# Performance work log

Measured on AMD Instinct MI355X. Metric: run time of the kernel, lower is better.

## Reference

```python
import jax, jax.numpy as jnp
import numpy as np
from jax import lax

NUM_EXPERTS = 64
HIDDEN = 1024
INTERMEDIATE = 768
TOTAL_TOKENS = 8192


def setup_inputs() -> dict:
    key = jax.random.key(0)
    k1, k2, k3, k4 = jax.random.split(key, 4)
    x = jax.random.normal(k1, (TOTAL_TOKENS, HIDDEN), dtype=jnp.float32)
    scale = 0.02
    w1 = jax.random.normal(k2, (NUM_EXPERTS, HIDDEN, INTERMEDIATE), dtype=jnp.float32) * scale
    w2 = jax.random.normal(k3, (NUM_EXPERTS, INTERMEDIATE, HIDDEN), dtype=jnp.float32) * scale
    w3 = jax.random.normal(k4, (NUM_EXPERTS, HIDDEN, INTERMEDIATE), dtype=jnp.float32) * scale
    # Variable tokens per expert, summing exactly to TOTAL_TOKENS (tokens are pre-sorted by expert).
    counts = np.random.default_rng(0).multinomial(TOTAL_TOKENS, [1.0 / NUM_EXPERTS] * NUM_EXPERTS)
    num_tokens_per_expert = jnp.asarray(counts, dtype=jnp.int32)
    return {"x": x, "w1": w1, "w2": w2, "w3": w3,
            "num_tokens_per_expert": num_tokens_per_expert}


def reference(x, w1, w2, w3, num_tokens_per_expert):
    """SwiGLU grouped-expert FFN: down(silu(gate(x)) * up(x)), grouped by expert.

    x: (T, H) tokens sorted by expert; num_tokens_per_expert: (E,) int32.
    Matches torch._grouped_mm semantics: compute in bfloat16, cast back to x.dtype.
    """
    gs = num_tokens_per_expert.astype(jnp.int32)
    xb = x.astype(jnp.bfloat16)
    w1b = w1.astype(jnp.bfloat16)
    w2b = w2.astype(jnp.bfloat16)
    w3b = w3.astype(jnp.bfloat16)
    gate = lax.ragged_dot(xb, w1b, gs)          # (T, I) grouped GEMM
    up = lax.ragged_dot(xb, w3b, gs)            # (T, I)
    h = jax.nn.silu(gate) * up                  # fused SwiGLU activation
    out = lax.ragged_dot(h, w2b, gs)            # (T, H)
    return out.astype(x.dtype)
```

## Files before the change

kernel.cpp:

```cpp
#include <hip/hip_runtime.h>
#include <stdint.h>

#define E_ 64
#define H_ 1024
#define I_ 768
#define T_ 8192

typedef __attribute__((ext_vector_type(4))) float floatx4;
typedef __attribute__((ext_vector_type(8))) short bf16x8;

__device__ inline unsigned short f2bf(float f) {
  union { float f; uint32_t u; } v; v.f = f;
  return (unsigned short)((v.u + 0x7FFFu + ((v.u >> 16) & 1u)) >> 16);
}
__device__ inline float bf2f(unsigned short s) {
  union { uint32_t u; float f; } v; v.u = ((uint32_t)s) << 16;
  return v.f;
}

__device__ inline void gload16(const void* g, void* l) {
  __builtin_amdgcn_global_load_lds(
      (const __attribute__((address_space(1))) void*)g,
      (__attribute__((address_space(3))) void*)l, 16, 0, 0);
}

__device__ inline int bslot(int n, int c) { return n * 4 + (c ^ ((n >> 1) & 3)); }

__global__ void k_prep(const float* __restrict__ x, unsigned short* __restrict__ xb,
                       const int* __restrict__ cnts, int* __restrict__ offs) {
  int i = blockIdx.x * 256 + threadIdx.x;
  float4 v = ((const float4*)x)[i];
  ushort4 o;
  o.x = f2bf(v.x); o.y = f2bf(v.y); o.z = f2bf(v.z); o.w = f2bf(v.w);
  ((ushort4*)xb)[i] = o;
  if (i == 0) {
    int s = 0; offs[0] = 0;
    for (int e = 0; e < E_; ++e) { s += cnts[e]; offs[e + 1] = s; }
  }
}

__global__ __launch_bounds__(256, 2) void k_gemm1(
    const unsigned short* __restrict__ xb, const float* __restrict__ w1,
    const float* __restrict__ w3, unsigned short* __restrict__ h,
    const int* __restrict__ offs) {
  __shared__ __align__(16) float Bf[2][2][32 * 64];
  __shared__ __align__(16) unsigned short Bh[2][64 * 32];

  const int tid = threadIdx.x;
  const int wv = tid >> 6;
  const int l = tid & 63;
  const int lq = l >> 4;
  const int ln = l & 15;
  const int bid = ((int)blockIdx.x & 7) * (E_ * (I_ / 64) / 8) + ((int)blockIdx.x >> 3);
  const int e = bid / (I_ / 64);
  const int n0 = (bid % (I_ / 64)) * 64;
  const int off = offs[e];
  const int cnt = offs[e + 1] - off;

  const int cn = tid & 63;
  const int ck = tid >> 6;

  const float* b1p = w1 + (size_t)e * (H_ * I_) + (size_t)(tid >> 4) * I_ + n0 + (tid & 15) * 4;
  const float* b3p = w3 + (size_t)e * (H_ * I_) + (size_t)(tid >> 4) * I_ + n0 + (tid & 15) * 4;

  for (int mb = 0; mb < cnt; mb += 256) {
    const int m_here = (cnt - mb) < 256 ? (cnt - mb) : 256;
    const bool active = (wv * 64) < m_here;

    const unsigned short* aF[4];
#pragma unroll
    for (int mf = 0; mf < 4; ++mf) {
      int row = off + mb + wv * 64 + mf * 16 + ln;
      row = row < (T_ - 1) ? row : (T_ - 1);
      aF[mf] = xb + (size_t)row * H_ + lq * 8;
    }

    auto STGB = [&](int kt, int buf) {
#pragma unroll
      for (int r = 0; r < 2; ++r) {
        gload16(b1p + (size_t)(kt * 32 + r * 16) * I_, &Bf[buf][0][tid * 4 + r * 1024]);
        gload16(b3p + (size_t)(kt * 32 + r * 16) * I_, &Bf[buf][1][tid * 4 + r * 1024]);
      }
    };

    floatx4 accG[4][4], accU[4][4];
#pragma unroll
    for (int i2 = 0; i2 < 4; ++i2)
#pragma unroll
      for (int j2 = 0; j2 < 4; ++j2) {
        accG[i2][j2] = (floatx4){0.f, 0.f, 0.f, 0.f};
        accU[i2][j2] = (floatx4){0.f, 0.f, 0.f, 0.f};
      }

    const int NK = H_ / 32;
    STGB(0, 0);
    STGB(1, 1);
    for (int kt = 0; kt < NK; ++kt) {
      const int cur = kt & 1;
      if (kt == NK - 1) asm volatile("s_waitcnt vmcnt(0)" ::: "memory");
      else              asm volatile("s_waitcnt vmcnt(4)" ::: "memory");
      __builtin_amdgcn_s_barrier();
      asm volatile("" ::: "memory");

#pragma unroll
      for (int m = 0; m < 2; ++m) {
        uint32_t dw[4];
#pragma unroll
        for (int d = 0; d < 4; ++d) {
          float v0 = Bf[cur][m][(ck * 8 + 2 * d) * 64 + cn];
          float v1 = Bf[cur][m][(ck * 8 + 2 * d + 1) * 64 + cn];
          dw[d] = (uint32_t)f2bf(v0) | ((uint32_t)f2bf(v1) << 16);
        }
        *(uint4*)&Bh[m][(size_t)bslot(cn, ck) * 8] = make_uint4(dw[0], dw[1], dw[2], dw[3]);
      }
      asm volatile("s_waitcnt lgkmcnt(0)" ::: "memory");
      __builtin_amdgcn_s_barrier();
      asm volatile("" ::: "memory");

      bf16x8 af[4];
      if (active) {
#pragma unroll
        for (int mf = 0; mf < 4; ++mf) af[mf] = *(const bf16x8*)(aF[mf] + kt * 32);
      }
      asm volatile("" ::: "memory");
      if (kt + 2 < NK) STGB(kt + 2, cur);
      asm volatile("" ::: "memory");

      if (active) {
        bf16x8 bG[4], bU[4];
#pragma unroll
        for (int nf = 0; nf < 4; ++nf) {
          const int sl = bslot(nf * 16 + ln, lq) * 8;
          bG[nf] = *(const bf16x8*)&Bh[0][sl];
          bU[nf] = *(const bf16x8*)&Bh[1][sl];
        }
#pragma unroll
        for (int mf = 0; mf < 4; ++mf)
#pragma unroll
          for (int nf = 0; nf < 4; ++nf) {
            accG[mf][nf] = __builtin_amdgcn_mfma_f32_16x16x32_bf16(af[mf], bG[nf], accG[mf][nf], 0, 0, 0);
            accU[mf][nf] = __builtin_amdgcn_mfma_f32_16x16x32_bf16(af[mf], bU[nf], accU[mf][nf], 0, 0, 0);
          }
      }
    }

    if (active) {
#pragma unroll
      for (int mf = 0; mf < 4; ++mf)
#pragma unroll
        for (int nf = 0; nf < 4; ++nf)
#pragma unroll
          for (int r = 0; r < 4; ++r) {
            int row_l = wv * 64 + mf * 16 + lq * 4 + r;
            if (row_l < m_here) {
              float g = bf2f(f2bf(accG[mf][nf][r]));
              float u = bf2f(f2bf(accU[mf][nf][r]));
              float hv = (g / (1.0f + __expf(-g))) * u;
              h[(size_t)(off + mb + row_l) * I_ + n0 + nf * 16 + ln] = f2bf(hv);
            }
          }
    }
    asm volatile("s_waitcnt vmcnt(0)" ::: "memory");
  }
}

__global__ __launch_bounds__(256, 3) void k_gemm2(
    const unsigned short* __restrict__ h, const float* __restrict__ w2,
    float* __restrict__ out, const int* __restrict__ offs) {
  __shared__ __align__(16) float Bf[2][32 * 64];
  __shared__ __align__(16) unsigned short Bh[64 * 32];

  const int tid = threadIdx.x;
  const int wv = tid >> 6;
  const int l = tid & 63;
  const int lq = l >> 4;
  const int ln = l & 15;
  const int bid = ((int)blockIdx.x & 7) * (E_ * (H_ / 64) / 8) + ((int)blockIdx.x >> 3);
  const int e = bid / (H_ / 64);
  const int n0 = (bid % (H_ / 64)) * 64;
  const int off = offs[e];
  const int cnt = offs[e + 1] - off;

  const int cn = tid & 63;
  const int ck = tid >> 6;

  const float* b2p = w2 + (size_t)e * (I_ * H_) + (size_t)(tid >> 4) * H_ + n0 + (tid & 15) * 4;

  for (int mb = 0; mb < cnt; mb += 256) {
    const int m_here = (cnt - mb) < 256 ? (cnt - mb) : 256;
    const bool active = (wv * 64) < m_here;

    const unsigned short* aF[4];
#pragma unroll
    for (int mf = 0; mf < 4; ++mf) {
      int row = off + mb + wv * 64 + mf * 16 + ln;
      row = row < (T_ - 1) ? row : (T_ - 1);
      aF[mf] = h + (size_t)row * I_ + lq * 8;
    }

    auto STGB = [&](int kt, int buf) {
#pragma unroll
      for (int r = 0; r < 2; ++r)
        gload16(b2p + (size_t)(kt * 32 + r * 16) * H_, &Bf[buf][tid * 4 + r * 1024]);
    };

    floatx4 acc[4][4];
#pragma unroll
    for (int i2 = 0; i2 < 4; ++i2)
#pragma unroll
      for (int j2 = 0; j2 < 4; ++j2) acc[i2][j2] = (floatx4){0.f, 0.f, 0.f, 0.f};

    const int NK = I_ / 32;
    STGB(0, 0);
    STGB(1, 1);
    for (int kt = 0; kt < NK; ++kt) {
      const int cur = kt & 1;
      if (kt == NK - 1) asm volatile("s_waitcnt vmcnt(0)" ::: "memory");
      else              asm volatile("s_waitcnt vmcnt(2)" ::: "memory");
      __builtin_amdgcn_s_barrier();
      asm volatile("" ::: "memory");

      {
        uint32_t dw[4];
#pragma unroll
        for (int d = 0; d < 4; ++d) {
          float v0 = Bf[cur][(ck * 8 + 2 * d) * 64 + cn];
          float v1 = Bf[cur][(ck * 8 + 2 * d + 1) * 64 + cn];
          dw[d] = (uint32_t)f2bf(v0) | ((uint32_t)f2bf(v1) << 16);
        }
        *(uint4*)&Bh[(size_t)bslot(cn, ck) * 8] = make_uint4(dw[0], dw[1], dw[2], dw[3]);
      }
      asm volatile("s_waitcnt lgkmcnt(0)" ::: "memory");
      __builtin_amdgcn_s_barrier();
      asm volatile("" ::: "memory");

      bf16x8 af[4];
      if (active) {
#pragma unroll
        for (int mf = 0; mf < 4; ++mf) af[mf] = *(const bf16x8*)(aF[mf] + kt * 32);
      }
      asm volatile("" ::: "memory");
      if (kt + 2 < NK) STGB(kt + 2, cur);
      asm volatile("" ::: "memory");

      if (active) {
        bf16x8 bF[4];
#pragma unroll
        for (int nf = 0; nf < 4; ++nf)
          bF[nf] = *(const bf16x8*)&Bh[(size_t)bslot(nf * 16 + ln, lq) * 8];
#pragma unroll
        for (int mf = 0; mf < 4; ++mf)
#pragma unroll
          for (int nf = 0; nf < 4; ++nf)
            acc[mf][nf] = __builtin_amdgcn_mfma_f32_16x16x32_bf16(af[mf], bF[nf], acc[mf][nf], 0, 0, 0);
      }
    }

    if (active) {
#pragma unroll
      for (int mf = 0; mf < 4; ++mf)
#pragma unroll
        for (int nf = 0; nf < 4; ++nf)
#pragma unroll
          for (int r = 0; r < 4; ++r) {
            int row_l = wv * 64 + mf * 16 + lq * 4 + r;
            if (row_l < m_here)
              out[(size_t)(off + mb + row_l) * H_ + n0 + nf * 16 + ln] = acc[mf][nf][r];
          }
    }
    asm volatile("s_waitcnt vmcnt(0)" ::: "memory");
  }
}

extern "C" void kernel_launch(void* const* d_in, const int* in_sizes, int n_in,
                              void* d_out, int out_size, void* d_ws, size_t ws_size,
                              hipStream_t stream) {
  const float* x  = (const float*)d_in[0];
  const float* w1 = (const float*)d_in[1];
  const float* w2 = (const float*)d_in[2];
  const float* w3 = (const float*)d_in[3];
  const int* cnts = (const int*)d_in[4];
  float* out = (float*)d_out;

  char* ws = (char*)d_ws;
  int* offs = (int*)ws;
  unsigned short* xb = (unsigned short*)(ws + 1024);
  unsigned short* h  = (unsigned short*)(ws + 1024 + (size_t)T_ * H_ * 2);

  k_prep<<<(T_ * H_) / (256 * 4), 256, 0, stream>>>(x, xb, cnts, offs);
  k_gemm1<<<E_ * (I_ / 64), 256, 0, stream>>>(xb, w1, w3, h, offs);
  k_gemm2<<<E_ * (H_ / 64), 256, 0, stream>>>(h, w2, out, offs);
}
```

Baseline: 619.3 us.

## Pre-convert weights to bf16 tiled layout and pipeline GEMMs with 4-stage buffers

A new prep kernel converts x to bf16 and also converts w1, w3 and w2 to bf16, written in an MFMA-ready tiled layout in workspace. The GEMM kernels then DMA bf16 tiles directly into a 4-deep LDS ring, with no in-loop fp32-to-bf16 conversion, only one barrier per k-step, and A fragments prefetched one step ahead. The goal is to remove per-tile conversion and LDS round trips from the GEMM inner loop. The cost is an extra pass that reads all fp32 weights and writes bf16 copies on every call, and a large workspace; if the workspace is too small, the old path runs.

```diff
diff --git a/kernel.cpp b/kernel.cpp
--- a/kernel.cpp
+++ b/kernel.cpp
@@ -24,20 +24,257 @@
       (__attribute__((address_space(3))) void*)l, 16, 0, 0);
 }
 
+__global__ void k_pt(const float* __restrict__ x, unsigned short* __restrict__ xb,
+                     const int* __restrict__ cnts, int* __restrict__ offs,
+                     const float* __restrict__ w1, const float* __restrict__ w3,
+                     const float* __restrict__ w2, unsigned short* __restrict__ w1t,
+                     unsigned short* __restrict__ w3t, unsigned short* __restrict__ w2t) {
+  const int tid = threadIdx.x;
+  const int b = blockIdx.x;
+  if (b < 8192) {
+    int i = b * 256 + tid;
+    float4 v = ((const float4*)x)[i];
+    ushort4 o;
+    o.x = f2bf(v.x); o.y = f2bf(v.y); o.z = f2bf(v.z); o.w = f2bf(v.w);
+    ((ushort4*)xb)[i] = o;
+    if (i == 0) {
+      int s = 0; offs[0] = 0;
+      for (int e = 0; e < E_; ++e) { s += cnts[e]; offs[e + 1] = s; }
+    }
+    return;
+  }
+  const int t2 = b - 8192;
+  const float* srcp; unsigned short* dstp; int N, KT, NB, idx;
+  if (t2 < 2048)      { srcp = w1; dstp = w1t; N = I_; KT = 32; NB = 12; idx = t2; }
+  else if (t2 < 4096) { srcp = w3; dstp = w3t; N = I_; KT = 32; NB = 12; idx = t2 - 2048; }
+  else                { srcp = w2; dstp = w2t; N = H_; KT = 24; NB = 16; idx = t2 - 4096; }
+  const int e = idx / KT, kt = idx % KT;
+  const int K = KT * 32;
+  const float* s0 = srcp + (size_t)e * K * N + (size_t)(kt * 32 + (tid & 3) * 8) * N + (tid >> 2);
+  unsigned short* d0 = dstp + ((size_t)e * NB * KT + kt) * 2048 + (size_t)tid * 8;
+  for (int nb = 0; nb < NB; ++nb) {
+    const float* s = s0 + nb * 64;
+    uint32_t dw[4];
+#pragma unroll
+    for (int d2 = 0; d2 < 4; ++d2) {
+      float v0 = s[(size_t)(2 * d2) * N];
+      float v1 = s[(size_t)(2 * d2 + 1) * N];
+      dw[d2] = (uint32_t)f2bf(v0) | ((uint32_t)f2bf(v1) << 16);
+    }
+    *(uint4*)(d0 + (size_t)nb * KT * 2048) = make_uint4(dw[0], dw[1], dw[2], dw[3]);
+  }
+}
+
+__global__ __launch_bounds__(256, 2) void k_gemm1_t(
+    const unsigned short* __restrict__ xb, const unsigned short* __restrict__ w1t,
+    const unsigned short* __restrict__ w3t, unsigned short* __restrict__ h,
+    const int* __restrict__ offs) {
+  __shared__ __align__(16) unsigned short Bh[4][2][2048];
+
+  const int tid = threadIdx.x;
+  const int wv = tid >> 6;
+  const int l = tid & 63;
+  const int lq = l >> 4;
+  const int ln = l & 15;
+  const int bid = ((int)blockIdx.x & 7) * (E_ * (I_ / 64) / 8) + ((int)blockIdx.x >> 3);
+  const int e = bid / (I_ / 64);
+  const int nb = bid % (I_ / 64);
+  const int n0 = nb * 64;
+  const int off = offs[e];
+  const int cnt = offs[e + 1] - off;
+
+  const unsigned short* w1s = w1t + (size_t)(e * 12 + nb) * (32 * 2048);
+  const unsigned short* w3s = w3t + (size_t)(e * 12 + nb) * (32 * 2048);
+  const int dmaOff = wv * 512 + l * 8;
+
+#define STGB1(kt)                                                            \
+  do {                                                                       \
+    int _b = (kt) & 3;                                                       \
+    gload16(w1s + (size_t)(kt) * 2048 + dmaOff, &Bh[_b][0][dmaOff]);         \
+    gload16(w3s + (size_t)(kt) * 2048 + dmaOff, &Bh[_b][1][dmaOff]);         \
+  } while (0)
+
+  for (int mb = 0; mb < cnt; mb += 256) {
+    const int m_here = (cnt - mb) < 256 ? (cnt - mb) : 256;
+    const bool active = (wv * 64) < m_here;
+
+    const unsigned short* aF[4];
+#pragma unroll
+    for (int mf = 0; mf < 4; ++mf) {
+      int row = off + mb + wv * 64 + mf * 16 + ln;
+      row = row < (T_ - 1) ? row : (T_ - 1);
+      aF[mf] = xb + (size_t)row * H_ + lq * 8;
+    }
+
+    floatx4 accG[4][4], accU[4][4];
+#pragma unroll
+    for (int i2 = 0; i2 < 4; ++i2)
+#pragma unroll
+      for (int j2 = 0; j2 < 4; ++j2) {
+        accG[i2][j2] = (floatx4){0.f, 0.f, 0.f, 0.f};
+        accU[i2][j2] = (floatx4){0.f, 0.f, 0.f, 0.f};
+      }
+
+    STGB1(0);
+    STGB1(1);
+    bf16x8 afA[4], afB[4];
+#pragma unroll
+    for (int mf = 0; mf < 4; ++mf) afA[mf] = *(const bf16x8*)(aF[mf]);
+
+#define STEP1(kt, cons, pref)                                                  \
+  do {                                                                         \
+    if ((kt) + 2 < 32) STGB1((kt) + 2);                                        \
+    if ((kt) + 1 < 32) {                                                       \
+      _Pragma("unroll") for (int mf = 0; mf < 4; ++mf)                         \
+          pref[mf] = *(const bf16x8*)(aF[mf] + ((kt) + 1) * 32);               \
+    }                                                                          \
+    asm volatile("s_waitcnt vmcnt(6)" ::: "memory");                           \
+    __builtin_amdgcn_s_barrier();                                              \
+    asm volatile("" ::: "memory");                                             \
+    const unsigned short* B0 = Bh[(kt) & 3][0];                                \
+    const unsigned short* B1 = Bh[(kt) & 3][1];                                \
+    if (active) {                                                              \
+      bf16x8 bG[4], bU[4];                                                     \
+      _Pragma("unroll") for (int nf = 0; nf < 4; ++nf) {                       \
+        int sl = ((nf * 16 + ln) * 4 + lq) * 8;                                \
+        bG[nf] = *(const bf16x8*)&B0[sl];                                      \
+        bU[nf] = *(const bf16x8*)&B1[sl];                                      \
+      }                                                                        \
+      _Pragma("unroll") for (int mf = 0; mf < 4; ++mf)                         \
+          _Pragma("unroll") for (int nf = 0; nf < 4; ++nf) {                   \
+        accG[mf][nf] =                                                         \
+            __builtin_amdgcn_mfma_f32_16x16x32_bf16(cons[mf], bG[nf],          \
+                                                    accG[mf][nf], 0, 0, 0);    \
+        accU[mf][nf] =                                                         \
+            __builtin_amdgcn_mfma_f32_16x16x32_bf16(cons[mf], bU[nf],          \
+                                                    accU[mf][nf], 0, 0, 0);    \
+      }                                                                        \
+    }                                                                          \
+    asm volatile("" ::: "memory");                                             \
+  } while (0)
+
+    for (int kt = 0; kt < 32; kt += 2) {
+      STEP1(kt, afA, afB);
+      STEP1(kt + 1, afB, afA);
+    }
+
+    if (active) {
+#pragma unroll
+      for (int mf = 0; mf < 4; ++mf)
+#pragma unroll
+        for (int nf = 0; nf < 4; ++nf)
+#pragma unroll
+          for (int r = 0; r < 4; ++r) {
+            int row_l = wv * 64 + mf * 16 + lq * 4 + r;
+            if (row_l < m_here) {
+              float g = bf2f(f2bf(accG[mf][nf][r]));
+              float u = bf2f(f2bf(accU[mf][nf][r]));
+              float hv = (g / (1.0f + __expf(-g))) * u;
+              h[(size_t)(off + mb + row_l) * I_ + n0 + nf * 16 + ln] = f2bf(hv);
+            }
+          }
+    }
+    asm volatile("s_waitcnt vmcnt(0)" ::: "memory");
+    __builtin_amdgcn_s_barrier();
+  }
+#undef STEP1
+#undef STGB1
+}
+
+__global__ __launch_bounds__(256, 2) void k_gemm2_t(
+    const unsigned short* __restrict__ h, const unsigned short* __restrict__ w2t,
+    float* __restrict__ out, const int* __restrict__ offs) {
+  __shared__ __align__(16) unsigned short Bh[4][2048];
+
+  const int tid = threadIdx.x;
+  const int wv = tid >> 6;
+  const int l = tid & 63;
+  const int lq = l >> 4;
+  const int ln = l & 15;
+  const int bid = ((int)blockIdx.x & 7) * (E_ * (H_ / 64) / 8) + ((int)blockIdx.x >> 3);
+  const int e = bid / (H_ / 64);
+  const int nb = bid % (H_ / 64);
+  const int n0 = nb * 64;
+  const int off = offs[e];
+  const int cnt = offs[e + 1] - off;
+
+  const unsigned short* w2s = w2t + (size_t)(e * 16 + nb) * (24 * 2048);
+  const int dmaOff = wv * 512 + l * 8;
+
+#define STGB2(kt) gload16(w2s + (size_t)(kt) * 2048 + dmaOff, &Bh[(kt) & 3][dmaOff])
+
+  for (int mb = 0; mb < cnt; mb += 256) {
+    const int m_here = (cnt - mb) < 256 ? (cnt - mb) : 256;
+    const bool active = (wv * 64) < m_here;
+
+    const unsigned short* aF[4];
+#pragma unroll
+    for (int mf = 0; mf < 4; ++mf) {
+      int row = off + mb + wv * 64 + mf * 16 + ln;
+      row = row < (T_ - 1) ? row : (T_ - 1);
+      aF[mf] = h + (size_t)row * I_ + lq * 8;
+    }
+
+    floatx4 acc[4][4];
+#pragma unroll
+    for (int i2 = 0; i2 < 4; ++i2)
+#pragma unroll
+      for (int j2 = 0; j2 < 4; ++j2) acc[i2][j2] = (floatx4){0.f, 0.f, 0.f, 0.f};
+
+    STGB2(0);
+    STGB2(1);
+    bf16x8 afA[4], afB[4];
+#pragma unroll
+    for (int mf = 0; mf < 4; ++mf) afA[mf] = *(const bf16x8*)(aF[mf]);
+
+#define STEP2(kt, cons, pref)                                                  \
+  do {                                                                         \
+    if ((kt) + 2 < 24) STGB2((kt) + 2);                                        \
+    if ((kt) + 1 < 24) {                                                       \
+      _Pragma("unroll") for (int mf = 0; mf < 4; ++mf)                         \
+          pref[mf] = *(const bf16x8*)(aF[mf] + ((kt) + 1) * 32);               \
+    }                                                                          \
+    asm volatile("s_waitcnt vmcnt(5)" ::: "memory");                           \
+    __builtin_amdgcn_s_barrier();                                              \
+    asm volatile("" ::: "memory");                                             \
+    const unsigned short* B0 = Bh[(kt) & 3];                                   \
+    if (active) {                                                              \
+      bf16x8 bF[4];                                                            \
+      _Pragma("unroll") for (int nf = 0; nf < 4; ++nf)                         \
+          bF[nf] = *(const bf16x8*)&B0[((nf * 16 + ln) * 4 + lq) * 8];         \
+      _Pragma("unroll") for (int mf = 0; mf < 4; ++mf)                         \
+          _Pragma("unroll") for (int nf = 0; nf < 4; ++nf)                     \
+              acc[mf][nf] = __builtin_amdgcn_mfma_f32_16x16x32_bf16(           \
+                  cons[mf], bF[nf], acc[mf][nf], 0, 0, 0);                     \
+    }                                                                          \
+    asm volatile("" ::: "memory");                                             \
+  } while (0)
+
+    for (int kt = 0; kt < 24; kt += 2) {
+      STEP2(kt, afA, afB);
+      STEP2(kt + 1, afB, afA);
+    }
+
+    if (active) {
+#pragma unroll
+      for (int mf = 0; mf < 4; ++mf)
+#pragma unroll
+        for (int nf = 0; nf < 4; ++nf)
+#pragma unroll
+          for (int r = 0; r < 4; ++r) {
+            int row_l = wv * 64 + mf * 16 + lq * 4 + r;
+            if (row_l < m_here)
+              out[(size_t)(off + mb + row_l) * H_ + n0 + nf * 16 + ln] = acc[mf][nf][r];
+          }
+    }
+    asm volatile("s_waitcnt vmcnt(0)" ::: "memory");
+    __builtin_amdgcn_s_barrier();
+  }
+#undef STEP2
+#undef STGB2
+}
+
 __device__ inline int bslot(int n, int c) { return n * 4 + (c ^ ((n >> 1) & 3)); }
-
-__global__ void k_prep(const float* __restrict__ x, unsigned short* __restrict__ xb,
-                       const int* __restrict__ cnts, int* __restrict__ offs) {
-  int i = blockIdx.x * 256 + threadIdx.x;
-  float4 v = ((const float4*)x)[i];
-  ushort4 o;
-  o.x = f2bf(v.x); o.y = f2bf(v.y); o.z = f2bf(v.z); o.w = f2bf(v.w);
-  ((ushort4*)xb)[i] = o;
-  if (i == 0) {
-    int s = 0; offs[0] = 0;
-    for (int e = 0; e < E_; ++e) { s += cnts[e]; offs[e + 1] = s; }
-  }
-}
 
 __global__ __launch_bounds__(256, 2) void k_gemm1(
     const unsigned short* __restrict__ xb, const float* __restrict__ w1,
@@ -56,17 +293,14 @@
   const int n0 = (bid % (I_ / 64)) * 64;
   const int off = offs[e];
   const int cnt = offs[e + 1] - off;
-
   const int cn = tid & 63;
   const int ck = tid >> 6;
-
   const float* b1p = w1 + (size_t)e * (H_ * I_) + (size_t)(tid >> 4) * I_ + n0 + (tid & 15) * 4;
   const float* b3p = w3 + (size_t)e * (H_ * I_) + (size_t)(tid >> 4) * I_ + n0 + (tid & 15) * 4;
 
   for (int mb = 0; mb < cnt; mb += 256) {
     const int m_here = (cnt - mb) < 256 ? (cnt - mb) : 256;
     const bool active = (wv * 64) < m_here;
-
     const unsigned short* aF[4];
 #pragma unroll
     for (int mf = 0; mf < 4; ++mf) {
@@ -74,7 +308,6 @@
       row = row < (T_ - 1) ? row : (T_ - 1);
       aF[mf] = xb + (size_t)row * H_ + lq * 8;
     }
-
     auto STGB = [&](int kt, int buf) {
 #pragma unroll
       for (int r = 0; r < 2; ++r) {
@@ -82,7 +315,6 @@
         gload16(b3p + (size_t)(kt * 32 + r * 16) * I_, &Bf[buf][1][tid * 4 + r * 1024]);
       }
     };
-
     floatx4 accG[4][4], accU[4][4];
 #pragma unroll
     for (int i2 = 0; i2 < 4; ++i2)
@@ -91,7 +323,6 @@
         accG[i2][j2] = (floatx4){0.f, 0.f, 0.f, 0.f};
         accU[i2][j2] = (floatx4){0.f, 0.f, 0.f, 0.f};
       }
-
     const int NK = H_ / 32;
     STGB(0, 0);
     STGB(1, 1);
@@ -101,7 +332,6 @@
       else              asm volatile("s_waitcnt vmcnt(4)" ::: "memory");
       __builtin_amdgcn_s_barrier();
       asm volatile("" ::: "memory");
-
 #pragma unroll
       for (int m = 0; m < 2; ++m) {
         uint32_t dw[4];
@@ -116,7 +346,6 @@
       asm volatile("s_waitcnt lgkmcnt(0)" ::: "memory");
       __builtin_amdgcn_s_barrier();
       asm volatile("" ::: "memory");
-
       bf16x8 af[4];
       if (active) {
 #pragma unroll
@@ -125,7 +354,6 @@
       asm volatile("" ::: "memory");
       if (kt + 2 < NK) STGB(kt + 2, cur);
       asm volatile("" ::: "memory");
-
       if (active) {
         bf16x8 bG[4], bU[4];
 #pragma unroll
@@ -143,7 +371,6 @@
           }
       }
     }
-
     if (active) {
 #pragma unroll
       for (int mf = 0; mf < 4; ++mf)
@@ -164,7 +391,7 @@
   }
 }
 
-__global__ __launch_bounds__(256, 3) void k_gemm2(
+__global__ __launch_bounds__(256, 2) void k_gemm2(
     const unsigned short* __restrict__ h, const float* __restrict__ w2,
     float* __restrict__ out, const int* __restrict__ offs) {
   __shared__ __align__(16) float Bf[2][32 * 64];
@@ -180,16 +407,13 @@
   const int n0 = (bid % (H_ / 64)) * 64;
   const int off = offs[e];
   const int cnt = offs[e + 1] - off;
-
   const int cn = tid & 63;
   const int ck = tid >> 6;
-
   const float* b2p = w2 + (size_t)e * (I_ * H_) + (size_t)(tid >> 4) * H_ + n0 + (tid & 15) * 4;
 
   for (int mb = 0; mb < cnt; mb += 256) {
     const int m_here = (cnt - mb) < 256 ? (cnt - mb) : 256;
     const bool active = (wv * 64) < m_here;
-
     const unsigned short* aF[4];
 #pragma unroll
     for (int mf = 0; mf < 4; ++mf) {
@@ -197,19 +421,16 @@
       row = row < (T_ - 1) ? row : (T_ - 1);
       aF[mf] = h + (size_t)row * I_ + lq * 8;
     }
-
     auto STGB = [&](int kt, int buf) {
 #pragma unroll
       for (int r = 0; r < 2; ++r)
         gload16(b2p + (size_t)(kt * 32 + r * 16) * H_, &Bf[buf][tid * 4 + r * 1024]);
     };
-
     floatx4 acc[4][4];
 #pragma unroll
     for (int i2 = 0; i2 < 4; ++i2)
 #pragma unroll
       for (int j2 = 0; j2 < 4; ++j2) acc[i2][j2] = (floatx4){0.f, 0.f, 0.f, 0.f};
-
     const int NK = I_ / 32;
     STGB(0, 0);
     STGB(1, 1);
@@ -219,7 +440,6 @@
       else              asm volatile("s_waitcnt vmcnt(2)" ::: "memory");
       __builtin_amdgcn_s_barrier();
       asm volatile("" ::: "memory");
-
       {
         uint32_t dw[4];
 #pragma unroll
@@ -233,7 +453,6 @@
       asm volatile("s_waitcnt lgkmcnt(0)" ::: "memory");
       __builtin_amdgcn_s_barrier();
       asm volatile("" ::: "memory");
-
       bf16x8 af[4];
       if (active) {
 #pragma unroll
@@ -242,7 +461,6 @@
       asm volatile("" ::: "memory");
       if (kt + 2 < NK) STGB(kt + 2, cur);
       asm volatile("" ::: "memory");
-
       if (active) {
         bf16x8 bF[4];
 #pragma unroll
@@ -255,7 +473,6 @@
             acc[mf][nf] = __builtin_amdgcn_mfma_f32_16x16x32_bf16(af[mf], bF[nf], acc[mf][nf], 0, 0, 0);
       }
     }
-
     if (active) {
 #pragma unroll
       for (int mf = 0; mf < 4; ++mf)
@@ -283,11 +500,24 @@
   float* out = (float*)d_out;
 
   char* ws = (char*)d_ws;
+  const size_t XB = (size_t)T_ * H_ * 2;
+  const size_t HB = (size_t)T_ * I_ * 2;
+  const size_t WT = (size_t)E_ * H_ * I_ * 2;
   int* offs = (int*)ws;
   unsigned short* xb = (unsigned short*)(ws + 1024);
-  unsigned short* h  = (unsigned short*)(ws + 1024 + (size_t)T_ * H_ * 2);
-
-  k_prep<<<(T_ * H_) / (256 * 4), 256, 0, stream>>>(x, xb, cnts, offs);
-  k_gemm1<<<E_ * (I_ / 64), 256, 0, stream>>>(xb, w1, w3, h, offs);
-  k_gemm2<<<E_ * (H_ / 64), 256, 0, stream>>>(h, w2, out, offs);
-}
+  unsigned short* h  = (unsigned short*)(ws + 1024 + XB);
+  const size_t need = 1024 + XB + HB + 3 * WT;
+
+  if (ws_size >= need) {
+    unsigned short* w1t = (unsigned short*)(ws + 1024 + XB + HB);
+    unsigned short* w3t = (unsigned short*)(ws + 1024 + XB + HB + WT);
+    unsigned short* w2t = (unsigned short*)(ws + 1024 + XB + HB + 2 * WT);
+    k_pt<<<8192 + 5632, 256, 0, stream>>>(x, xb, cnts, offs, w1, w3, w2, w1t, w3t, w2t);
+    k_gemm1_t<<<E_ * (I_ / 64), 256, 0, stream>>>(xb, w1t, w3t, h, offs);
+    k_gemm2_t<<<E_ * (H_ / 64), 256, 0, stream>>>(h, w2t, out, offs);
+  } else {
+    k_pt<<<8192, 256, 0, stream>>>(x, xb, cnts, offs, w1, w3, w2, xb, xb, xb);
+    k_gemm1<<<E_ * (I_ / 64), 256, 0, stream>>>(xb, w1, w3, h, offs);
+    k_gemm2<<<E_ * (H_ / 64), 256, 0, stream>>>(h, w2, out, offs);
+  }
+}
```

New measurement: 758.9 us. +22.5%, slower.
